# Kernel tuning notes

Measured on AMD Instinct MI355X. Metric: run time of the kernel, lower is better.

Reference implementation:

```python
import jax, jax.numpy as jnp
import numpy as np

N_EMBED = 256
HEAD_SIZE = 64
B, T = 32, 768

def setup_inputs() -> dict:
    key = jax.random.key(0)
    kx, kq, kk, kv = jax.random.split(key, 4)
    bound = 1.0 / np.sqrt(N_EMBED)  # torch nn.Linear default init
    return {
        "x": jax.random.normal(kx, (B, T, N_EMBED), dtype=jnp.float32),
        "wq": jax.random.uniform(kq, (N_EMBED, HEAD_SIZE), minval=-bound, maxval=bound, dtype=jnp.float32),
        "wk": jax.random.uniform(kk, (N_EMBED, HEAD_SIZE), minval=-bound, maxval=bound, dtype=jnp.float32),
        "wv": jax.random.uniform(kv, (N_EMBED, HEAD_SIZE), minval=-bound, maxval=bound, dtype=jnp.float32),
    }

def reference(x, wq, wk, wv):
    # x: [B, T, C]; wq/wk/wv: [C, H]
    q = jnp.einsum('btc,ch->bth', x, wq)
    k = jnp.einsum('btc,ch->bth', x, wk)
    v = jnp.einsum('btc,ch->bth', x, wv)
    scale = k.shape[-1] ** -0.5
    scores = jnp.einsum('bqh,bkh->bqk', q, k) * scale  # [B, T, T]
    Tn = x.shape[1]
    causal = jnp.tril(jnp.ones((Tn, Tn), dtype=bool))
    scores = jnp.where(causal, scores, -jnp.inf)
    attn = jax.nn.softmax(scores, axis=-1)
    # dropout omitted (eval mode) for deterministic reference
    return jnp.einsum('bqk,bkh->bqh', attn, v)
```

## Files before the change

### kernel.cpp

```cpp
#include <hip/hip_runtime.h>
#include <hip/hip_bf16.h>

#define B_  32
#define T_  768
#define C_  256
#define H_  64
#define BT_ (B_*T_)

using short8 = __attribute__((ext_vector_type(8))) short;
using f32x4  = __attribute__((ext_vector_type(4))) float;

__device__ __forceinline__ ushort f2bf(float f) {
    union { float f; unsigned u; } v; v.f = f;
    unsigned u = v.u;
    return (ushort)((u + 0x7FFFu + ((u >> 16) & 1u)) >> 16);
}

__global__ __launch_bounds__(256) void qkv_proj_kernel(
    const float* __restrict__ x, const float* __restrict__ wq,
    const float* __restrict__ wk, const float* __restrict__ wv,
    ushort* __restrict__ qkv)
{
    __shared__ ushort wT[64][264];
    const int tid   = threadIdx.x;
    const int wv_id = tid >> 6;
    const int lane  = tid & 63;
    const int g     = lane >> 4;
    const int c     = lane & 15;
    const int row   = blockIdx.x*64 + wv_id*16 + c;

    short8 a[8];
    const float* xr = x + row*C_;
    #pragma unroll
    for (int ch = 0; ch < 8; ++ch) {
        const float4 f0 = *(const float4*)(xr + ch*32 + g*8);
        const float4 f1 = *(const float4*)(xr + ch*32 + g*8 + 4);
        short8 t;
        t[0]=(short)f2bf(f0.x); t[1]=(short)f2bf(f0.y); t[2]=(short)f2bf(f0.z); t[3]=(short)f2bf(f0.w);
        t[4]=(short)f2bf(f1.x); t[5]=(short)f2bf(f1.y); t[6]=(short)f2bf(f1.z); t[7]=(short)f2bf(f1.w);
        a[ch] = t;
    }

    for (int m = 0; m < 3; ++m) {
        const float* wsrc = (m == 0) ? wq : ((m == 1) ? wk : wv);
        for (int i = tid; i < C_*H_; i += 256)
            wT[i & 63][i >> 6] = f2bf(wsrc[i]);
        __syncthreads();

        ushort* dst = qkv + m*BT_*H_ + (blockIdx.x*64 + wv_id*16)*H_;
        #pragma unroll
        for (int jn = 0; jn < 4; ++jn) {
            f32x4 acc = {0.f, 0.f, 0.f, 0.f};
            #pragma unroll
            for (int ch = 0; ch < 8; ++ch) {
                const short8 bw = *(const short8*)(&wT[jn*16 + c][ch*32 + g*8]);
                acc = __builtin_amdgcn_mfma_f32_16x16x32_bf16(a[ch], bw, acc, 0, 0, 0);
            }
            #pragma unroll
            for (int r = 0; r < 4; ++r)
                dst[(g*4 + r)*H_ + jn*16 + c] = f2bf(acc[r]);
        }
        __syncthreads();
    }
}

__global__ __launch_bounds__(256) void attn_kernel(
    const ushort* __restrict__ qkv, float* __restrict__ out)
{
    __shared__ ushort vT [64][72];
    __shared__ ushort pls[4][16][72];

    const int tid   = threadIdx.x;
    const int wv_id = tid >> 6;
    const int lane  = tid & 63;
    const int g     = lane >> 4;
    const int c     = lane & 15;
    const int qt    = 11 - (blockIdx.x >> 5);
    const int b     = blockIdx.x & 31;

    const ushort* kbase = qkv + BT_*H_;
    const ushort* vbase = qkv + 2*BT_*H_;

    short8 aq[2];
    const ushort* qp = qkv + (b*T_ + qt*64 + wv_id*16 + c)*H_;
    #pragma unroll
    for (int ch = 0; ch < 2; ++ch)
        aq[ch] = *(const short8*)(qp + ch*32 + g*8);

    float m_[4], l_[4];
    f32x4 o[4];
    #pragma unroll
    for (int r = 0; r < 4; ++r) { m_[r] = -INFINITY; l_[r] = 0.f; }
    #pragma unroll
    for (int jh = 0; jh < 4; ++jh) o[jh] = (f32x4){0.f, 0.f, 0.f, 0.f};

    for (int kt = 0; kt <= qt; ++kt) {
        __syncthreads();
        const ushort* vsrc = vbase + (b*T_ + kt*64)*H_;
        #pragma unroll
        for (int it = 0; it < 2; ++it) {
            const int i   = tid + it*256;
            const int r   = i >> 3;
            const int seg = (i & 7) * 8;
            const short8 u = *(const short8*)(vsrc + r*H_ + seg);
            #pragma unroll
            for (int e = 0; e < 8; ++e) vT[seg + e][r] = (ushort)u[e];
        }
        __syncthreads();

        f32x4 s[4];
        #pragma unroll
        for (int j = 0; j < 4; ++j) {
            f32x4 acc = {0.f, 0.f, 0.f, 0.f};
            #pragma unroll
            for (int ch = 0; ch < 2; ++ch) {
                const short8 bk = *(const short8*)(kbase + (b*T_ + kt*64 + j*16 + c)*H_ + ch*32 + g*8);
                acc = __builtin_amdgcn_mfma_f32_16x16x32_bf16(aq[ch], bk, acc, 0, 0, 0);
            }
            s[j] = acc;
        }

        const bool diag = (kt == qt);
        #pragma unroll
        for (int j = 0; j < 4; ++j) {
            #pragma unroll
            for (int r = 0; r < 4; ++r) {
                float v = s[j][r] * 0.125f;
                if (diag && (j*16 + c > wv_id*16 + g*4 + r)) v = -1e30f;
                s[j][r] = v;
            }
        }

        #pragma unroll
        for (int r = 0; r < 4; ++r) {
            float tm = fmaxf(fmaxf(s[0][r], s[1][r]), fmaxf(s[2][r], s[3][r]));
            tm = fmaxf(tm, __shfl_xor(tm, 1));
            tm = fmaxf(tm, __shfl_xor(tm, 2));
            tm = fmaxf(tm, __shfl_xor(tm, 4));
            tm = fmaxf(tm, __shfl_xor(tm, 8));
            const float mn = fmaxf(m_[r], tm);
            const float al = __expf(m_[r] - mn);
            m_[r] = mn;
            float ps = 0.f;
            #pragma unroll
            for (int j = 0; j < 4; ++j) {
                const float p = __expf(s[j][r] - mn);
                s[j][r] = p;
                ps += p;
            }
            ps += __shfl_xor(ps, 1);
            ps += __shfl_xor(ps, 2);
            ps += __shfl_xor(ps, 4);
            ps += __shfl_xor(ps, 8);
            l_[r] = l_[r]*al + ps;
            #pragma unroll
            for (int jh = 0; jh < 4; ++jh) o[jh][r] *= al;
        }

        #pragma unroll
        for (int j = 0; j < 4; ++j) {
            #pragma unroll
            for (int r = 0; r < 4; ++r)
                pls[wv_id][g*4 + r][j*16 + c] = f2bf(s[j][r]);
        }

        #pragma unroll
        for (int c2 = 0; c2 < 2; ++c2) {
            const short8 ap = *(const short8*)(&pls[wv_id][c][c2*32 + g*8]);
            #pragma unroll
            for (int jh = 0; jh < 4; ++jh) {
                const short8 bv = *(const short8*)(&vT[jh*16 + c][c2*32 + g*8]);
                o[jh] = __builtin_amdgcn_mfma_f32_16x16x32_bf16(ap, bv, o[jh], 0, 0, 0);
            }
        }
    }

    float* op = out + (b*T_ + qt*64 + wv_id*16)*H_;
    #pragma unroll
    for (int jh = 0; jh < 4; ++jh) {
        #pragma unroll
        for (int r = 0; r < 4; ++r)
            op[(g*4 + r)*H_ + jh*16 + c] = o[jh][r] / l_[r];
    }
}

extern "C" void kernel_launch(void* const* d_in, const int* in_sizes, int n_in,
                              void* d_out, int out_size, void* d_ws, size_t ws_size,
                              hipStream_t stream) {
    const float* x  = (const float*)d_in[0];
    const float* wq = (const float*)d_in[1];
    const float* wk = (const float*)d_in[2];
    const float* wv = (const float*)d_in[3];
    ushort* qkv = (ushort*)d_ws;

    qkv_proj_kernel<<<dim3(BT_/64), dim3(256), 0, stream>>>(x, wq, wk, wv, qkv);
    attn_kernel<<<dim3(B_*12), dim3(256), 0, stream>>>(qkv, (float*)d_out);
}
```

Baseline: 122.1 us.

## Pre-transpose weights, store V transposed, double-buffer K/V tiles in attention

Adds a small kernel that converts and transposes the three weight matrices to bf16 once, so each projection block stops re-reading the fp32 weights with strided transposing LDS writes. The projection now stages its outputs through LDS and writes them out coalesced, with V stored transposed so the attention kernel no longer transposes V in LDS. The attention kernel stages K and V tiles in double-buffered LDS, prefetching the next tile into registers while computing on the current one. This costs an extra launch, more LDS per block and extra barriers.

```diff
diff --git a/kernel.cpp b/kernel.cpp
--- a/kernel.cpp
+++ b/kernel.cpp
@@ -6,6 +6,7 @@
 #define C_  256
 #define H_  64
 #define BT_ (B_*T_)
+#define WT_OFF (3*BT_*H_)
 
 using short8 = __attribute__((ext_vector_type(8))) short;
 using f32x4  = __attribute__((ext_vector_type(4))) float;
@@ -16,18 +17,30 @@
     return (ushort)((u + 0x7FFFu + ((u >> 16) & 1u)) >> 16);
 }
 
+__global__ __launch_bounds__(256) void prep_w_kernel(
+    const float* __restrict__ wq, const float* __restrict__ wk,
+    const float* __restrict__ wv, ushort* __restrict__ ws)
+{
+    const int idx = blockIdx.x*256 + threadIdx.x;
+    const int m = idx >> 14, r = idx & 16383;
+    const int h = r >> 8, k = r & 255;
+    const float* w = (m == 0) ? wq : (m == 1) ? wk : wv;
+    ws[WT_OFF + idx] = f2bf(w[k*H_ + h]);
+}
+
 __global__ __launch_bounds__(256) void qkv_proj_kernel(
-    const float* __restrict__ x, const float* __restrict__ wq,
-    const float* __restrict__ wk, const float* __restrict__ wv,
-    ushort* __restrict__ qkv)
+    const float* __restrict__ x, ushort* __restrict__ ws)
 {
     __shared__ ushort wT[64][264];
+    __shared__ ushort vls[64][72];
     const int tid   = threadIdx.x;
     const int wv_id = tid >> 6;
     const int lane  = tid & 63;
     const int g     = lane >> 4;
     const int c     = lane & 15;
-    const int row   = blockIdx.x*64 + wv_id*16 + c;
+    const int rowbase = blockIdx.x*64;
+    const int row     = rowbase + wv_id*16 + c;
+    const int sh = tid >> 2, ss = tid & 3;
 
     short8 a[8];
     const float* xr = x + row*C_;
@@ -41,13 +54,13 @@
         a[ch] = t;
     }
 
+    const ushort* wtg = ws + WT_OFF;
+    #pragma unroll
+    for (int i = 0; i < 8; ++i)
+        *(short8*)&wT[sh][ss*64 + i*8] = *(const short8*)(wtg + sh*256 + ss*64 + i*8);
+    __syncthreads();
+
     for (int m = 0; m < 3; ++m) {
-        const float* wsrc = (m == 0) ? wq : ((m == 1) ? wk : wv);
-        for (int i = tid; i < C_*H_; i += 256)
-            wT[i & 63][i >> 6] = f2bf(wsrc[i]);
-        __syncthreads();
-
-        ushort* dst = qkv + m*BT_*H_ + (blockIdx.x*64 + wv_id*16)*H_;
         #pragma unroll
         for (int jn = 0; jn < 4; ++jn) {
             f32x4 acc = {0.f, 0.f, 0.f, 0.f};
@@ -56,18 +69,39 @@
                 const short8 bw = *(const short8*)(&wT[jn*16 + c][ch*32 + g*8]);
                 acc = __builtin_amdgcn_mfma_f32_16x16x32_bf16(a[ch], bw, acc, 0, 0, 0);
             }
-            #pragma unroll
-            for (int r = 0; r < 4; ++r)
-                dst[(g*4 + r)*H_ + jn*16 + c] = f2bf(acc[r]);
+            if (m < 2) {
+                #pragma unroll
+                for (int r = 0; r < 4; ++r)
+                    vls[wv_id*16 + g*4 + r][jn*16 + c] = f2bf(acc[r]);
+            } else {
+                #pragma unroll
+                for (int r = 0; r < 4; ++r)
+                    vls[jn*16 + c][wv_id*16 + g*4 + r] = f2bf(acc[r]);
+            }
         }
         __syncthreads();
+        {
+            ushort* dst = (m < 2)
+                ? (ws + m*BT_*H_ + (rowbase + sh)*H_ + ss*16)
+                : (ws + 2*BT_*H_ + sh*BT_ + rowbase + ss*16);
+            *(short8*)(dst)     = *(const short8*)&vls[sh][ss*16];
+            *(short8*)(dst + 8) = *(const short8*)&vls[sh][ss*16 + 8];
+            if (m < 2) {
+                const ushort* src = wtg + (m+1)*16384 + sh*256 + ss*64;
+                #pragma unroll
+                for (int i = 0; i < 8; ++i)
+                    *(short8*)&wT[sh][ss*64 + i*8] = *(const short8*)(src + i*8);
+            }
+        }
+        __syncthreads();
     }
 }
 
 __global__ __launch_bounds__(256) void attn_kernel(
-    const ushort* __restrict__ qkv, float* __restrict__ out)
+    const ushort* __restrict__ ws, float* __restrict__ out)
 {
-    __shared__ ushort vT [64][72];
+    __shared__ ushort kls[2][64][72];
+    __shared__ ushort vls[2][64][72];
     __shared__ ushort pls[4][16][72];
 
     const int tid   = threadIdx.x;
@@ -77,15 +111,16 @@
     const int c     = lane & 15;
     const int qt    = 11 - (blockIdx.x >> 5);
     const int b     = blockIdx.x & 31;
-
-    const ushort* kbase = qkv + BT_*H_;
-    const ushort* vbase = qkv + 2*BT_*H_;
+    const int nkt   = qt + 1;
+    const int sh = tid >> 2, ss = tid & 3;
+
+    const ushort* kg  = ws + BT_*H_ + b*T_*H_;
+    const ushort* vtg = ws + 2*BT_*H_ + b*T_;
 
     short8 aq[2];
-    const ushort* qp = qkv + (b*T_ + qt*64 + wv_id*16 + c)*H_;
-    #pragma unroll
-    for (int ch = 0; ch < 2; ++ch)
-        aq[ch] = *(const short8*)(qp + ch*32 + g*8);
+    const ushort* qp = ws + (b*T_ + qt*64 + wv_id*16 + c)*H_;
+    aq[0] = *(const short8*)(qp + g*8);
+    aq[1] = *(const short8*)(qp + 32 + g*8);
 
     float m_[4], l_[4];
     f32x4 o[4];
@@ -94,19 +129,28 @@
     #pragma unroll
     for (int jh = 0; jh < 4; ++jh) o[jh] = (f32x4){0.f, 0.f, 0.f, 0.f};
 
-    for (int kt = 0; kt <= qt; ++kt) {
-        __syncthreads();
-        const ushort* vsrc = vbase + (b*T_ + kt*64)*H_;
-        #pragma unroll
-        for (int it = 0; it < 2; ++it) {
-            const int i   = tid + it*256;
-            const int r   = i >> 3;
-            const int seg = (i & 7) * 8;
-            const short8 u = *(const short8*)(vsrc + r*H_ + seg);
-            #pragma unroll
-            for (int e = 0; e < 8; ++e) vT[seg + e][r] = (ushort)u[e];
-        }
-        __syncthreads();
+    short8 kreg0, kreg1, vreg0, vreg1;
+    #define LOAD_TILES(kt_) do { \
+        const ushort* ksrc = kg + ((kt_)*64 + sh)*H_ + ss*16;       \
+        kreg0 = *(const short8*)ksrc; kreg1 = *(const short8*)(ksrc + 8); \
+        const ushort* vsrc = vtg + sh*BT_ + (kt_)*64 + ss*16;       \
+        vreg0 = *(const short8*)vsrc; vreg1 = *(const short8*)(vsrc + 8); \
+    } while (0)
+    #define WRITE_TILES(bi_) do { \
+        *(short8*)&kls[bi_][sh][ss*16]     = kreg0; \
+        *(short8*)&kls[bi_][sh][ss*16 + 8] = kreg1; \
+        *(short8*)&vls[bi_][sh][ss*16]     = vreg0; \
+        *(short8*)&vls[bi_][sh][ss*16 + 8] = vreg1; \
+    } while (0)
+
+    LOAD_TILES(0);
+    WRITE_TILES(0);
+    __syncthreads();
+
+    int cur = 0;
+    for (int kt = 0; kt < nkt; ++kt) {
+        const bool more = (kt + 1 < nkt);
+        if (more) LOAD_TILES(kt + 1);
 
         f32x4 s[4];
         #pragma unroll
@@ -114,7 +158,7 @@
             f32x4 acc = {0.f, 0.f, 0.f, 0.f};
             #pragma unroll
             for (int ch = 0; ch < 2; ++ch) {
-                const short8 bk = *(const short8*)(kbase + (b*T_ + kt*64 + j*16 + c)*H_ + ch*32 + g*8);
+                const short8 bk = *(const short8*)(&kls[cur][j*16 + c][ch*32 + g*8]);
                 acc = __builtin_amdgcn_mfma_f32_16x16x32_bf16(aq[ch], bk, acc, 0, 0, 0);
             }
             s[j] = acc;
@@ -169,19 +213,26 @@
             const short8 ap = *(const short8*)(&pls[wv_id][c][c2*32 + g*8]);
             #pragma unroll
             for (int jh = 0; jh < 4; ++jh) {
-                const short8 bv = *(const short8*)(&vT[jh*16 + c][c2*32 + g*8]);
+                const short8 bv = *(const short8*)(&vls[cur][jh*16 + c][c2*32 + g*8]);
                 o[jh] = __builtin_amdgcn_mfma_f32_16x16x32_bf16(ap, bv, o[jh], 0, 0, 0);
             }
         }
+
+        if (more) WRITE_TILES(cur ^ 1);
+        __syncthreads();
+        cur ^= 1;
     }
 
     float* op = out + (b*T_ + qt*64 + wv_id*16)*H_;
     #pragma unroll
-    for (int jh = 0; jh < 4; ++jh) {
-        #pragma unroll
-        for (int r = 0; r < 4; ++r)
-            op[(g*4 + r)*H_ + jh*16 + c] = o[jh][r] / l_[r];
-    }
+    for (int r = 0; r < 4; ++r) {
+        const float inv = 1.0f / l_[r];
+        #pragma unroll
+        for (int jh = 0; jh < 4; ++jh)
+            op[(g*4 + r)*H_ + jh*16 + c] = o[jh][r] * inv;
+    }
+    #undef LOAD_TILES
+    #undef WRITE_TILES
 }
 
 extern "C" void kernel_launch(void* const* d_in, const int* in_sizes, int n_in,
@@ -191,8 +242,9 @@
     const float* wq = (const float*)d_in[1];
     const float* wk = (const float*)d_in[2];
     const float* wv = (const float*)d_in[3];
-    ushort* qkv = (ushort*)d_ws;
-
-    qkv_proj_kernel<<<dim3(BT_/64), dim3(256), 0, stream>>>(x, wq, wk, wv, qkv);
-    attn_kernel<<<dim3(B_*12), dim3(256), 0, stream>>>(qkv, (float*)d_out);
-}
+    ushort* ws = (ushort*)d_ws;
+
+    prep_w_kernel<<<dim3(192), dim3(256), 0, stream>>>(wq, wk, wv, ws);
+    qkv_proj_kernel<<<dim3(BT_/64), dim3(256), 0, stream>>>(x, ws);
+    attn_kernel<<<dim3(B_*12), dim3(256), 0, stream>>>(ws, (float*)d_out);
+}
```

After: 108.9 us. 10.8% less time.
